# Kernel tuning notes

Hardware: AMD Instinct MI355X
Metric: run time of the kernel (lower is better)

The kernel has to match this reference:

```python
import jax, jax.numpy as jnp
import numpy as np

B, S, D, H, DK = 2, 2048, 2048, 16, 128


def setup_inputs() -> dict:
    key = jax.random.key(0)
    k1, k2, k3 = jax.random.split(key, 3)
    hidden_states = jax.random.normal(k1, (B, S, D), dtype=jnp.float32)
    # causal multiplicative 0/1 mask [b, s, m]
    causal = jnp.tril(jnp.ones((S, S), dtype=jnp.float32))
    attention_mask = jnp.broadcast_to(causal, (B, S, S))
    qkv = jax.random.normal(k2, (D, 3, H, DK), dtype=jnp.float32) * (D ** -0.5)
    o = jax.random.normal(k3, (H, DK, D), dtype=jnp.float32) * ((H * DK) ** -0.5)
    return {"hidden_states": hidden_states, "attention_mask": attention_mask, "qkv": qkv, "o": o}


def reference(hidden_states, attention_mask, qkv, o):
    d_kernel = qkv.shape[-1]
    # _split2: project to q, k, v -> [b, h, s, dk]
    qkv_proj = jnp.einsum("bsc,cqhk->bqhsk", hidden_states, qkv)
    q, k, v = qkv_proj[:, 0], qkv_proj[:, 1], qkv_proj[:, 2]
    umask = attention_mask[:, None, :, :]  # [b, 1, s, m]
    scores = jnp.einsum("bhsk,bhmk->bhsm", q, k) * (d_kernel ** -0.5)
    scores = scores * umask - (1.0 - umask) * 10000.0
    probs = jnp.exp(jax.nn.log_softmax(scores, axis=-1))
    out = jnp.einsum("bhsm,bhmk->bshk", probs, v)
    out = jnp.einsum("bshk,hkc->bsc", out, o)
    return out
```

## Files before the change

kernel.cpp:

```cpp
#include <hip/hip_runtime.h>
#include <stdint.h>

typedef __attribute__((ext_vector_type(8))) short bf16x8;
typedef __attribute__((ext_vector_type(4))) float f32x4;
typedef __attribute__((ext_vector_type(4))) short s16x4;
typedef unsigned int u32;

#define MFMA_B16(a, b, c) __builtin_amdgcn_mfma_f32_16x16x32_bf16((a), (b), (c), 0, 0, 0)

__device__ __forceinline__ short f2b(float f) {
  u32 u = __builtin_bit_cast(u32, f);
  u32 r = (u + 0x7fffu + ((u >> 16) & 1u)) >> 16;
  return (short)(r & 0xffffu);
}

__device__ __forceinline__ void gload16(const void* g, void* l) {
  __builtin_amdgcn_global_load_lds((const __attribute__((address_space(1))) u32*)g,
                                   (__attribute__((address_space(3))) u32*)l, 16, 0, 0);
}

__device__ __forceinline__ bf16x8 rdfrag(const char* half, int row, int ks, int g) {
  int x = row * 128 + ((ks * 64 + g * 16) ^ ((row & 7) << 4));
  return *(const bf16x8*)(half + x);
}

__global__ __launch_bounds__(256) void k_f32_to_bf16(const float* __restrict__ in,
                                                     short* __restrict__ out, int n4) {
  int i = blockIdx.x * 256 + threadIdx.x;
  if (i < n4) {
    float4 v = ((const float4*)in)[i];
    s16x4 o;
    o.x = f2b(v.x); o.y = f2b(v.y); o.z = f2b(v.z); o.w = f2b(v.w);
    ((s16x4*)out)[i] = o;
  }
}

__global__ __launch_bounds__(256) void k_transpose_bf16(const float* __restrict__ in,
                                                        short* __restrict__ out, int R, int C) {
  __shared__ short tile[32][33];
  int tx = threadIdx.x, ty = threadIdx.y;
  int x = blockIdx.x * 32 + tx;
  int y0 = blockIdx.y * 32;
#pragma unroll
  for (int k = 0; k < 4; k++)
    tile[ty + 8 * k][tx] = f2b(in[(size_t)(y0 + ty + 8 * k) * C + x]);
  __syncthreads();
  int ox = y0 + tx;
#pragma unroll
  for (int k = 0; k < 4; k++)
    out[(size_t)(blockIdx.x * 32 + ty + 8 * k) * R + ox] = tile[tx][ty + 8 * k];
}

#define STG(dstbase, Pan, hrow0, kt_)                                                    \
  do {                                                                                   \
    gload16((Pan) + (size_t)((hrow0) + srow0) * 4096 + (size_t)(kt_) * 128 + skb0,       \
            (char*)lds + (dstbase) + w * 1024);                                          \
    gload16((Pan) + (size_t)((hrow0) + 64 + srow0) * 4096 + (size_t)(kt_) * 128 + skb0,  \
            (char*)lds + (dstbase) + 8192 + w * 1024);                                   \
  } while (0)

template <int CUR>
__device__ __forceinline__ void tile_step(char* lds, const char* APan, const char* BPan, int T,
                                          int w, int wr, int wc, int g, int c, int brb,
                                          int srow0, int skb0, f32x4 (&acc)[8][4]) {
  const char* hA = (const char*)lds + CUR * 65536 + wr * 16384;
  const char* hB = (const char*)lds + CUR * 65536 + 32768 + (wc >> 1) * 16384;
  const int oA = (CUR ^ 1) * 65536;
  bf16x8 a[4][2], b0[2][2], b1[2][2];

#pragma unroll
  for (int mi = 0; mi < 4; mi++)
#pragma unroll
    for (int ks = 0; ks < 2; ks++) a[mi][ks] = rdfrag(hA, mi * 16 + c, ks, g);
#pragma unroll
  for (int ni = 0; ni < 2; ni++)
#pragma unroll
    for (int ks = 0; ks < 2; ks++) b0[ni][ks] = rdfrag(hB, brb + ni * 16 + c, ks, g);
  STG(oA, APan, 0, T + 1);
  STG(oA + 16384, APan, 128, T + 1);
  asm volatile("s_waitcnt lgkmcnt(8)" ::: "memory");
  __builtin_amdgcn_s_barrier();
  asm volatile("s_waitcnt lgkmcnt(0)" ::: "memory");
  __builtin_amdgcn_sched_barrier(0);
  __builtin_amdgcn_s_setprio(1);
#pragma unroll
  for (int mi = 0; mi < 4; mi++)
#pragma unroll
    for (int ni = 0; ni < 2; ni++)
#pragma unroll
      for (int ks = 0; ks < 2; ks++) acc[mi][ni] = MFMA_B16(a[mi][ks], b0[ni][ks], acc[mi][ni]);
  __builtin_amdgcn_s_setprio(0);
  __builtin_amdgcn_s_barrier();

#pragma unroll
  for (int mi = 0; mi < 4; mi++)
#pragma unroll
    for (int ks = 0; ks < 2; ks++) a[mi][ks] = rdfrag(hA, 64 + mi * 16 + c, ks, g);
  __builtin_amdgcn_s_barrier();
  asm volatile("s_waitcnt lgkmcnt(0)" ::: "memory");
  __builtin_amdgcn_sched_barrier(0);
  __builtin_amdgcn_s_setprio(1);
#pragma unroll
  for (int mi = 0; mi < 4; mi++)
#pragma unroll
    for (int ni = 0; ni < 2; ni++)
#pragma unroll
      for (int ks = 0; ks < 2; ks++)
        acc[4 + mi][ni] = MFMA_B16(a[mi][ks], b0[ni][ks], acc[4 + mi][ni]);
  __builtin_amdgcn_s_setprio(0);
  __builtin_amdgcn_s_barrier();

#pragma unroll
  for (int ni = 0; ni < 2; ni++)
#pragma unroll
    for (int ks = 0; ks < 2; ks++) b1[ni][ks] = rdfrag(hB, brb + 32 + ni * 16 + c, ks, g);
  __builtin_amdgcn_s_barrier();
  asm volatile("s_waitcnt lgkmcnt(0)" ::: "memory");
  __builtin_amdgcn_sched_barrier(0);
  __builtin_amdgcn_s_setprio(1);
#pragma unroll
  for (int mi = 0; mi < 4; mi++)
#pragma unroll
    for (int ni = 0; ni < 2; ni++)
#pragma unroll
      for (int ks = 0; ks < 2; ks++)
        acc[4 + mi][2 + ni] = MFMA_B16(a[mi][ks], b1[ni][ks], acc[4 + mi][2 + ni]);
  __builtin_amdgcn_s_setprio(0);
  __builtin_amdgcn_s_barrier();

#pragma unroll
  for (int mi = 0; mi < 4; mi++)
#pragma unroll
    for (int ks = 0; ks < 2; ks++) a[mi][ks] = rdfrag(hA, mi * 16 + c, ks, g);
  STG(CUR * 65536 + 32768, BPan, 0, T + 2);
  STG(CUR * 65536 + 49152, BPan, 128, T + 2);
  __builtin_amdgcn_s_barrier();
  asm volatile("s_waitcnt lgkmcnt(0)" ::: "memory");
  __builtin_amdgcn_sched_barrier(0);
  __builtin_amdgcn_s_setprio(1);
#pragma unroll
  for (int mi = 0; mi < 4; mi++)
#pragma unroll
    for (int ni = 0; ni < 2; ni++)
#pragma unroll
      for (int ks = 0; ks < 2; ks++)
        acc[mi][2 + ni] = MFMA_B16(a[mi][ks], b1[ni][ks], acc[mi][2 + ni]);
  __builtin_amdgcn_s_setprio(0);
  asm volatile("s_waitcnt vmcnt(4)" ::: "memory");
  __builtin_amdgcn_s_barrier();
}

template <int EPI>
__global__ __launch_bounds__(512, 2) void gemm_8ph(const short* __restrict__ A,
                                                   const short* __restrict__ BT,
                                                   void* __restrict__ out0) {
  __shared__ char lds[131072];
  const int tid = threadIdx.x;
  const int w = tid >> 6, lane = tid & 63;
  const int g = lane >> 4, c = lane & 15;
  const int wr = w >> 2, wc = w & 3;
  const int brb = (wc & 1) * 64;

  const int nbx = gridDim.x;
  const int id0 = blockIdx.y * nbx + blockIdx.x;
  const int per = (nbx * gridDim.y) >> 3;
  const int nid = (id0 & 7) * per + (id0 >> 3);
  const int by = nid / nbx, bx2 = nid - by * nbx;
  const int m0 = by * 256, n0 = bx2 * 256;

  const char* APan = (const char*)(A + (size_t)m0 * 2048);
  const char* BPan = (const char*)(BT + (size_t)n0 * 2048);

  const int srow0 = tid >> 3;
  const int skb0 = ((tid & 7) * 16) ^ ((srow0 & 7) << 4);

  f32x4 acc[8][4] = {};

  STG(0, APan, 0, 0);
  STG(16384, APan, 128, 0);
  STG(32768, BPan, 0, 0);
  STG(49152, BPan, 128, 0);
  STG(65536 + 32768, BPan, 0, 1);
  STG(65536 + 49152, BPan, 128, 1);
  asm volatile("s_waitcnt vmcnt(4)" ::: "memory");
  __builtin_amdgcn_s_barrier();

  for (int it = 0; it < 16; ++it) {
    tile_step<0>(lds, APan, BPan, 2 * it, w, wr, wc, g, c, brb, srow0, skb0, acc);
    tile_step<1>(lds, APan, BPan, 2 * it + 1, w, wr, wc, g, c, brb, srow0, skb0, acc);
  }
  asm volatile("s_waitcnt vmcnt(0)" ::: "memory");

  if (EPI == 0) {
    short* Qb = (short*)out0;
    short* Kb = Qb + 8388608;
    short* Vt = Qb + 16777216;
#pragma unroll
    for (int ni = 0; ni < 4; ni++) {
      int n = n0 + wc * 64 + ni * 16 + c;
      int qq = n >> 11, hh = (n >> 7) & 15, dk = n & 127;
#pragma unroll
      for (int mi = 0; mi < 8; mi++) {
#pragma unroll
        for (int r = 0; r < 4; r++) {
          int m = m0 + wr * 128 + mi * 16 + g * 4 + r;
          int b_ = m >> 11, s = m & 2047;
          int bh = b_ * 16 + hh;
          short bv = f2b(acc[mi][ni][r]);
          if (qq == 0)
            Qb[((size_t)bh * 2048 + s) * 128 + dk] = bv;
          else if (qq == 1)
            Kb[((size_t)bh * 2048 + s) * 128 + dk] = bv;
          else
            Vt[((size_t)bh * 128 + dk) * 2048 + s] = bv;
        }
      }
    }
  } else {
    float* Co = (float*)out0;
#pragma unroll
    for (int ni = 0; ni < 4; ni++) {
      int n = n0 + wc * 64 + ni * 16 + c;
#pragma unroll
      for (int mi = 0; mi < 8; mi++) {
#pragma unroll
        for (int r = 0; r < 4; r++) {
          int m = m0 + wr * 128 + mi * 16 + g * 4 + r;
          Co[(size_t)m * 2048 + n] = acc[mi][ni][r];
        }
      }
    }
  }
}

__global__ __launch_bounds__(256, 2) void attn_fwd(const short* __restrict__ Qb,
                                                   const short* __restrict__ Kb,
                                                   const short* __restrict__ VTb,
                                                   short* __restrict__ Ob) {
  __shared__ short Ks[64 * 128];
  __shared__ short Vs[128 * 64];
  __shared__ short Ps[4][16][72];
  const int tid = threadIdx.x, w = tid >> 6, lane = tid & 63;
  const int g = lane >> 4, c = lane & 15;

  const int id0 = blockIdx.y * gridDim.x + blockIdx.x;
  const int nid = (id0 & 7) * 64 + (id0 >> 3);
  const int bx = nid & 15, bh = nid >> 4;

  const short* Qg = Qb + (size_t)bh * 2048 * 128;
  const short* Kg = Kb + (size_t)bh * 2048 * 128;
  const short* Vg = VTb + (size_t)bh * 128 * 2048;
  const int b = bh >> 4, hh = bh & 15;
  const float scale = 0.08838834764831845f;

  for (int pass = 0; pass < 2; ++pass) {
    const int qi = pass ? 31 - bx : bx;
    const int qs = qi * 64;

    bf16x8 qf[4];
    const int qrow = qs + w * 16 + c;
#pragma unroll
    for (int kc = 0; kc < 4; kc++)
      qf[kc] = *(const bf16x8*)(Qg + (size_t)qrow * 128 + kc * 32 + g * 8);

    float m_r[4], l_r[4];
    f32x4 accO[8];
#pragma unroll
    for (int r = 0; r < 4; r++) { m_r[r] = -INFINITY; l_r[r] = 0.f; }
#pragma unroll
    for (int nt = 0; nt < 8; nt++) accO[nt] = (f32x4){0.f, 0.f, 0.f, 0.f};

    for (int j = 0; j <= qi; ++j) {
      const int js = j * 64;
#pragma unroll
      for (int i = 0; i < 4; i++) {
        int ch = i * 256 + tid;
        {
          int row = ch >> 4, ci = ch & 15;
          int cis = ci ^ (row & 7);
          gload16(Kg + (size_t)(js + row) * 128 + cis * 8, (char*)Ks + i * 4096 + w * 1024);
        }
        {
          int row = ch >> 3, ci = ch & 7;
          int cis = ci ^ (row & 7);
          gload16(Vg + (size_t)row * 2048 + js + cis * 8, (char*)Vs + i * 4096 + w * 1024);
        }
      }
      __syncthreads();

      f32x4 accS[4] = {};
      __builtin_amdgcn_s_setprio(1);
#pragma unroll
      for (int t = 0; t < 4; t++) {
#pragma unroll
        for (int kc = 0; kc < 4; kc++) {
          int row = t * 16 + c;
          int kbyte = (kc * 64 + g * 16) ^ ((row & 7) << 4);
          bf16x8 kf = *(const bf16x8*)((const char*)Ks + row * 256 + kbyte);
          accS[t] = MFMA_B16(qf[kc], kf, accS[t]);
        }
      }
      __builtin_amdgcn_s_setprio(0);

      const bool diag = (j == qi);
      float sv[4][4];
#pragma unroll
      for (int t = 0; t < 4; t++)
#pragma unroll
        for (int r = 0; r < 4; r++) {
          float v = accS[t][r] * scale;
          if (diag) {
            int mcol = js + t * 16 + c;
            int srow = qs + w * 16 + g * 4 + r;
            if (mcol > srow) v = -1e30f;
          }
          sv[t][r] = v;
        }

#pragma unroll
      for (int r = 0; r < 4; r++) {
        float mx = fmaxf(fmaxf(sv[0][r], sv[1][r]), fmaxf(sv[2][r], sv[3][r]));
#pragma unroll
        for (int o = 8; o >= 1; o >>= 1) mx = fmaxf(mx, __shfl_xor(mx, o));
        if (mx - m_r[r] > 8.f) {
          float mnew = fmaxf(m_r[r], mx);
          float alpha = __expf(m_r[r] - mnew);
          l_r[r] *= alpha;
#pragma unroll
          for (int nt = 0; nt < 8; nt++) accO[nt][r] *= alpha;
          m_r[r] = mnew;
        }
        float rs = 0.f;
#pragma unroll
        for (int t = 0; t < 4; t++) {
          float p = __expf(sv[t][r] - m_r[r]);
          sv[t][r] = p;
          rs += p;
        }
#pragma unroll
        for (int o = 8; o >= 1; o >>= 1) rs += __shfl_xor(rs, o);
        l_r[r] += rs;
      }

#pragma unroll
      for (int t = 0; t < 4; t++)
#pragma unroll
        for (int r = 0; r < 4; r++) Ps[w][g * 4 + r][t * 16 + c] = f2b(sv[t][r]);

      __builtin_amdgcn_s_setprio(1);
#pragma unroll
      for (int kc2 = 0; kc2 < 2; kc2++) {
        bf16x8 pf = *(const bf16x8*)(&Ps[w][c][kc2 * 32 + g * 8]);
#pragma unroll
        for (int nt = 0; nt < 8; nt++) {
          int row = nt * 16 + c;
          int mbyte = (kc2 * 64 + g * 16) ^ ((row & 7) << 4);
          bf16x8 vf = *(const bf16x8*)((const char*)Vs + row * 128 + mbyte);
          accO[nt] = MFMA_B16(pf, vf, accO[nt]);
        }
      }
      __builtin_amdgcn_s_setprio(0);
      __syncthreads();
    }

#pragma unroll
    for (int r = 0; r < 4; r++) {
      float inv = 1.f / l_r[r];
      int s = qs + w * 16 + g * 4 + r;
      size_t base = ((size_t)b * 2048 + s) * 2048 + hh * 128;
#pragma unroll
      for (int nt = 0; nt < 8; nt++) {
        int kcol = nt * 16 + c;
        Ob[base + kcol] = f2b(accO[nt][r] * inv);
      }
    }
  }
}

extern "C" void kernel_launch(void* const* d_in, const int* in_sizes, int n_in, void* d_out,
                              int out_size, void* d_ws, size_t ws_size, hipStream_t stream) {
  (void)in_sizes; (void)n_in; (void)out_size; (void)ws_size;
  const float* hidden = (const float*)d_in[0];
  const float* qkvw = (const float*)d_in[2];
  const float* ow = (const float*)d_in[3];

  char* ws = (char*)d_ws;
  short* hiddenB = (short*)(ws);
  short* qkvT = (short*)(ws + 16777216);
  short* oT = (short*)(ws + 16777216);
  short* Qb = (short*)(ws + 41943040);
  short* attnO = (short*)(ws);

  k_f32_to_bf16<<<dim3(8192), dim3(256), 0, stream>>>(hidden, hiddenB, 2097152);
  k_transpose_bf16<<<dim3(192, 64), dim3(32, 8), 0, stream>>>(qkvw, qkvT, 2048, 6144);
  gemm_8ph<0><<<dim3(24, 16), dim3(512), 0, stream>>>(hiddenB, qkvT, (void*)Qb);
  k_transpose_bf16<<<dim3(64, 64), dim3(32, 8), 0, stream>>>(ow, oT, 2048, 2048);
  attn_fwd<<<dim3(16, 32), dim3(256), 0, stream>>>(Qb, Qb + 8388608, Qb + 16777216, attnO);
  gemm_8ph<1><<<dim3(8, 16), dim3(512), 0, stream>>>(attnO, oT, d_out);
}
```

Baseline: 450.0 us.

## Restructure GEMM into two-phase tile step and halve N-tile for output projection

Result: faster. 427.1 us (-5.1%).

```diff
diff --git a/kernel.cpp b/kernel.cpp
--- a/kernel.cpp
+++ b/kernel.cpp
@@ -51,33 +51,33 @@
     out[(size_t)(blockIdx.x * 32 + ty + 8 * k) * R + ox] = tile[tx][ty + 8 * k];
 }
 
-#define STG(dstbase, Pan, hrow0, kt_)                                                    \
-  do {                                                                                   \
-    gload16((Pan) + (size_t)((hrow0) + srow0) * 4096 + (size_t)(kt_) * 128 + skb0,       \
-            (char*)lds + (dstbase) + w * 1024);                                          \
-    gload16((Pan) + (size_t)((hrow0) + 64 + srow0) * 4096 + (size_t)(kt_) * 128 + skb0,  \
-            (char*)lds + (dstbase) + 8192 + w * 1024);                                   \
-  } while (0)
-
-template <int CUR>
+#define STG1(dstbase, Pan, hrow0, kt_)                                                  \
+  gload16((Pan) + (size_t)((hrow0) + srow0) * 4096 + (size_t)(kt_) * 128 + skb0,        \
+          (char*)lds + (dstbase) + w * 1024)
+
+template <int NQ, int CUR>
 __device__ __forceinline__ void tile_step(char* lds, const char* APan, const char* BPan, int T,
                                           int w, int wr, int wc, int g, int c, int brb,
-                                          int srow0, int skb0, f32x4 (&acc)[8][4]) {
-  const char* hA = (const char*)lds + CUR * 65536 + wr * 16384;
-  const char* hB = (const char*)lds + CUR * 65536 + 32768 + (wc >> 1) * 16384;
-  const int oA = (CUR ^ 1) * 65536;
-  bf16x8 a[4][2], b0[2][2], b1[2][2];
+                                          int srow0, int skb0, f32x4 (&acc)[8][NQ]) {
+  constexpr int HB = NQ * 4096;
+  constexpr int BUFSZ = 32768 + 2 * HB;
+  const char* hA = (const char*)lds + CUR * BUFSZ + wr * 16384;
+  const char* hB = (const char*)lds + CUR * BUFSZ + 32768 + (wc >> 1) * HB;
+  const int oA = (CUR ^ 1) * BUFSZ;
+  bf16x8 a[4][2], b[NQ][2];
 
 #pragma unroll
   for (int mi = 0; mi < 4; mi++)
 #pragma unroll
     for (int ks = 0; ks < 2; ks++) a[mi][ks] = rdfrag(hA, mi * 16 + c, ks, g);
 #pragma unroll
-  for (int ni = 0; ni < 2; ni++)
-#pragma unroll
-    for (int ks = 0; ks < 2; ks++) b0[ni][ks] = rdfrag(hB, brb + ni * 16 + c, ks, g);
-  STG(oA, APan, 0, T + 1);
-  STG(oA + 16384, APan, 128, T + 1);
+  for (int ni = 0; ni < NQ; ni++)
+#pragma unroll
+    for (int ks = 0; ks < 2; ks++) b[ni][ks] = rdfrag(hB, brb + ni * 16 + c, ks, g);
+  STG1(oA, APan, 0, T + 1);
+  STG1(oA + 8192, APan, 64, T + 1);
+  STG1(oA + 16384, APan, 128, T + 1);
+  STG1(oA + 24576, APan, 192, T + 1);
   asm volatile("s_waitcnt lgkmcnt(8)" ::: "memory");
   __builtin_amdgcn_s_barrier();
   asm volatile("s_waitcnt lgkmcnt(0)" ::: "memory");
@@ -86,9 +86,9 @@
 #pragma unroll
   for (int mi = 0; mi < 4; mi++)
 #pragma unroll
-    for (int ni = 0; ni < 2; ni++)
-#pragma unroll
-      for (int ks = 0; ks < 2; ks++) acc[mi][ni] = MFMA_B16(a[mi][ks], b0[ni][ks], acc[mi][ni]);
+    for (int ni = 0; ni < NQ; ni++)
+#pragma unroll
+      for (int ks = 0; ks < 2; ks++) acc[mi][ni] = MFMA_B16(a[mi][ks], b[ni][ks], acc[mi][ni]);
   __builtin_amdgcn_s_setprio(0);
   __builtin_amdgcn_s_barrier();
 
@@ -96,6 +96,11 @@
   for (int mi = 0; mi < 4; mi++)
 #pragma unroll
     for (int ks = 0; ks < 2; ks++) a[mi][ks] = rdfrag(hA, 64 + mi * 16 + c, ks, g);
+#pragma unroll
+  for (int h = 0; h < 2; h++)
+#pragma unroll
+    for (int j = 0; j < NQ / 2; j++)
+      STG1(CUR * BUFSZ + 32768 + h * HB + j * 8192, BPan, h * NQ * 32 + j * 64, T + 2);
   __builtin_amdgcn_s_barrier();
   asm volatile("s_waitcnt lgkmcnt(0)" ::: "memory");
   __builtin_amdgcn_sched_barrier(0);
@@ -103,70 +108,34 @@
 #pragma unroll
   for (int mi = 0; mi < 4; mi++)
 #pragma unroll
-    for (int ni = 0; ni < 2; ni++)
+    for (int ni = 0; ni < NQ; ni++)
 #pragma unroll
       for (int ks = 0; ks < 2; ks++)
-        acc[4 + mi][ni] = MFMA_B16(a[mi][ks], b0[ni][ks], acc[4 + mi][ni]);
+        acc[4 + mi][ni] = MFMA_B16(a[mi][ks], b[ni][ks], acc[4 + mi][ni]);
   __builtin_amdgcn_s_setprio(0);
-  __builtin_amdgcn_s_barrier();
-
-#pragma unroll
-  for (int ni = 0; ni < 2; ni++)
-#pragma unroll
-    for (int ks = 0; ks < 2; ks++) b1[ni][ks] = rdfrag(hB, brb + 32 + ni * 16 + c, ks, g);
-  __builtin_amdgcn_s_barrier();
-  asm volatile("s_waitcnt lgkmcnt(0)" ::: "memory");
-  __builtin_amdgcn_sched_barrier(0);
-  __builtin_amdgcn_s_setprio(1);
-#pragma unroll
-  for (int mi = 0; mi < 4; mi++)
-#pragma unroll
-    for (int ni = 0; ni < 2; ni++)
-#pragma unroll
-      for (int ks = 0; ks < 2; ks++)
-        acc[4 + mi][2 + ni] = MFMA_B16(a[mi][ks], b1[ni][ks], acc[4 + mi][2 + ni]);
-  __builtin_amdgcn_s_setprio(0);
-  __builtin_amdgcn_s_barrier();
-
-#pragma unroll
-  for (int mi = 0; mi < 4; mi++)
-#pragma unroll
-    for (int ks = 0; ks < 2; ks++) a[mi][ks] = rdfrag(hA, mi * 16 + c, ks, g);
-  STG(CUR * 65536 + 32768, BPan, 0, T + 2);
-  STG(CUR * 65536 + 49152, BPan, 128, T + 2);
-  __builtin_amdgcn_s_barrier();
-  asm volatile("s_waitcnt lgkmcnt(0)" ::: "memory");
-  __builtin_amdgcn_sched_barrier(0);
-  __builtin_amdgcn_s_setprio(1);
-#pragma unroll
-  for (int mi = 0; mi < 4; mi++)
-#pragma unroll
-    for (int ni = 0; ni < 2; ni++)
-#pragma unroll
-      for (int ks = 0; ks < 2; ks++)
-        acc[mi][2 + ni] = MFMA_B16(a[mi][ks], b1[ni][ks], acc[mi][2 + ni]);
-  __builtin_amdgcn_s_setprio(0);
-  asm volatile("s_waitcnt vmcnt(4)" ::: "memory");
-  __builtin_amdgcn_s_barrier();
-}
-
-template <int EPI>
-__global__ __launch_bounds__(512, 2) void gemm_8ph(const short* __restrict__ A,
+  asm volatile("s_waitcnt vmcnt(%0)" ::"i"(NQ) : "memory");
+  __builtin_amdgcn_s_barrier();
+}
+
+template <int EPI, int NQ>
+__global__ __launch_bounds__(512, 2) void gemm_2ph(const short* __restrict__ A,
                                                    const short* __restrict__ BT,
                                                    void* __restrict__ out0) {
-  __shared__ char lds[131072];
+  constexpr int HB = NQ * 4096;
+  constexpr int BUFSZ = 32768 + 2 * HB;
+  __shared__ char lds[2 * BUFSZ];
   const int tid = threadIdx.x;
   const int w = tid >> 6, lane = tid & 63;
   const int g = lane >> 4, c = lane & 15;
   const int wr = w >> 2, wc = w & 3;
-  const int brb = (wc & 1) * 64;
+  const int brb = (wc & 1) * (NQ * 16);
 
   const int nbx = gridDim.x;
   const int id0 = blockIdx.y * nbx + blockIdx.x;
   const int per = (nbx * gridDim.y) >> 3;
   const int nid = (id0 & 7) * per + (id0 >> 3);
   const int by = nid / nbx, bx2 = nid - by * nbx;
-  const int m0 = by * 256, n0 = bx2 * 256;
+  const int m0 = by * 256, n0 = bx2 * (NQ * 64);
 
   const char* APan = (const char*)(A + (size_t)m0 * 2048);
   const char* BPan = (const char*)(BT + (size_t)n0 * 2048);
@@ -174,20 +143,25 @@
   const int srow0 = tid >> 3;
   const int skb0 = ((tid & 7) * 16) ^ ((srow0 & 7) << 4);
 
-  f32x4 acc[8][4] = {};
-
-  STG(0, APan, 0, 0);
-  STG(16384, APan, 128, 0);
-  STG(32768, BPan, 0, 0);
-  STG(49152, BPan, 128, 0);
-  STG(65536 + 32768, BPan, 0, 1);
-  STG(65536 + 49152, BPan, 128, 1);
-  asm volatile("s_waitcnt vmcnt(4)" ::: "memory");
+  f32x4 acc[8][NQ] = {};
+
+  STG1(0, APan, 0, 0);
+  STG1(8192, APan, 64, 0);
+  STG1(16384, APan, 128, 0);
+  STG1(24576, APan, 192, 0);
+#pragma unroll
+  for (int h = 0; h < 2; h++)
+#pragma unroll
+    for (int j = 0; j < NQ / 2; j++) {
+      STG1(32768 + h * HB + j * 8192, BPan, h * NQ * 32 + j * 64, 0);
+      STG1(BUFSZ + 32768 + h * HB + j * 8192, BPan, h * NQ * 32 + j * 64, 1);
+    }
+  asm volatile("s_waitcnt vmcnt(%0)" ::"i"(NQ) : "memory");
   __builtin_amdgcn_s_barrier();
 
   for (int it = 0; it < 16; ++it) {
-    tile_step<0>(lds, APan, BPan, 2 * it, w, wr, wc, g, c, brb, srow0, skb0, acc);
-    tile_step<1>(lds, APan, BPan, 2 * it + 1, w, wr, wc, g, c, brb, srow0, skb0, acc);
+    tile_step<NQ, 0>(lds, APan, BPan, 2 * it, w, wr, wc, g, c, brb, srow0, skb0, acc);
+    tile_step<NQ, 1>(lds, APan, BPan, 2 * it + 1, w, wr, wc, g, c, brb, srow0, skb0, acc);
   }
   asm volatile("s_waitcnt vmcnt(0)" ::: "memory");
 
@@ -196,8 +170,8 @@
     short* Kb = Qb + 8388608;
     short* Vt = Qb + 16777216;
 #pragma unroll
-    for (int ni = 0; ni < 4; ni++) {
-      int n = n0 + wc * 64 + ni * 16 + c;
+    for (int ni = 0; ni < NQ; ni++) {
+      int n = n0 + wc * (NQ * 16) + ni * 16 + c;
       int qq = n >> 11, hh = (n >> 7) & 15, dk = n & 127;
 #pragma unroll
       for (int mi = 0; mi < 8; mi++) {
@@ -219,8 +193,8 @@
   } else {
     float* Co = (float*)out0;
 #pragma unroll
-    for (int ni = 0; ni < 4; ni++) {
-      int n = n0 + wc * 64 + ni * 16 + c;
+    for (int ni = 0; ni < NQ; ni++) {
+      int n = n0 + wc * (NQ * 16) + ni * 16 + c;
 #pragma unroll
       for (int mi = 0; mi < 8; mi++) {
 #pragma unroll
@@ -393,8 +367,8 @@
 
   k_f32_to_bf16<<<dim3(8192), dim3(256), 0, stream>>>(hidden, hiddenB, 2097152);
   k_transpose_bf16<<<dim3(192, 64), dim3(32, 8), 0, stream>>>(qkvw, qkvT, 2048, 6144);
-  gemm_8ph<0><<<dim3(24, 16), dim3(512), 0, stream>>>(hiddenB, qkvT, (void*)Qb);
+  gemm_2ph<0, 4><<<dim3(24, 16), dim3(512), 0, stream>>>(hiddenB, qkvT, (void*)Qb);
   k_transpose_bf16<<<dim3(64, 64), dim3(32, 8), 0, stream>>>(ow, oT, 2048, 2048);
   attn_fwd<<<dim3(16, 32), dim3(256), 0, stream>>>(Qb, Qb + 8388608, Qb + 16777216, attnO);
-  gemm_8ph<1><<<dim3(8, 16), dim3(512), 0, stream>>>(attnO, oT, d_out);
-}
+  gemm_2ph<1, 2><<<dim3(16, 16), dim3(512), 0, stream>>>(attnO, oT, d_out);
+}
```
